# Performance work log

Measured on AMD Instinct MI355X. Metric: run time of the kernel, lower is better.

The kernel has to match this reference:

```python
import jax, jax.numpy as jnp
import numpy as np

D_MODEL, D_K, D_V, H, M = 1024, 64, 64, 16, 40


def setup_inputs() -> dict:
    key = jax.random.key(0)
    ks = jax.random.split(key, 16)
    b, nq, nk = 8, 1024, 1024
    inp = {
        "queries": jax.random.normal(ks[0], (b, nq, D_MODEL), jnp.float32),
        "keys": jax.random.normal(ks[1], (b, nk, D_MODEL), jnp.float32),
        "values": jax.random.normal(ks[2], (b, nk, D_MODEL), jnp.float32),
        "attention_mask": jax.random.randint(ks[3], (b, H, nq, nk), 0, 2) > 0,
        # Linear params, parametrized as x @ W + b (W has shape (in, out)).
        "Wq": jax.random.normal(ks[4], (D_MODEL, H * D_K), jnp.float32) * 0.03,
        "bq": jnp.zeros((H * D_K,), jnp.float32),
        "Wk": jax.random.normal(ks[5], (D_MODEL, H * D_K), jnp.float32) * 0.03,
        "bk": jnp.zeros((H * D_K,), jnp.float32),
        "Wv": jax.random.normal(ks[6], (D_MODEL, H * D_V), jnp.float32) * 0.03,
        "bv": jnp.zeros((H * D_V,), jnp.float32),
        "Wo": jax.random.normal(ks[7], (H * D_V, D_MODEL), jnp.float32) * 0.03,
        "bo": jnp.zeros((D_MODEL,), jnp.float32),
        # Memory slots: m_k ~ N(0, 1/d_k), m_v ~ N(0, 1/m), shape (1, m, h*d)
        "m_k": jax.random.normal(ks[8], (1, M, H * D_K), jnp.float32) / D_K,
        "m_v": jax.random.normal(ks[9], (1, M, H * D_V), jnp.float32) / M,
    }
    return inp


def reference(queries, keys, values, attention_mask, Wq, bq, Wk, bk, Wv, bv, Wo, bo, m_k, m_v):
    b, nq, _ = queries.shape
    nk = keys.shape[1]
    scale = jnp.asarray(np.sqrt(D_K), jnp.float32)

    # scaled memory slots, broadcast over batch
    mk = scale * jnp.broadcast_to(m_k, (b, M, H * D_K))
    mv = jnp.asarray(np.sqrt(M), jnp.float32) * jnp.broadcast_to(m_v, (b, M, H * D_V))

    q = (queries @ Wq + bq).reshape(b, nq, H, D_K).transpose(0, 2, 1, 3)       # b h nq dk
    k = jnp.concatenate([keys @ Wk + bk, mk], axis=1)                           # b (nk+m) h*dk
    k = k.reshape(b, nk + M, H, D_K).transpose(0, 2, 1, 3)                      # b h (nk+m) dk
    v = jnp.concatenate([values @ Wv + bv, mv], axis=1)
    v = v.reshape(b, nk + M, H, D_V).transpose(0, 2, 1, 3)                      # b h (nk+m) dv

    att = jnp.einsum('bhqd,bhkd->bhqk', q, k) / scale                           # b h nq (nk+m)
    # mask only real keys; memory slots always attendable
    att_real = jnp.where(attention_mask, -jnp.inf, att[:, :, :, :nk])
    att = jnp.concatenate([att_real, att[:, :, :, nk:]], axis=-1)
    att = jax.nn.softmax(att, axis=-1)

    out = jnp.einsum('bhqk,bhkd->bhqd', att, v)
    out = out.transpose(0, 2, 1, 3).reshape(b, nq, H * D_V)
    out = out @ Wo + bo
    return out, att
```

## Files before the change

kernel.cpp:

```cpp
#include <hip/hip_runtime.h>
#include <hip/hip_bf16.h>


#define B_ 8
#define NQ 1024
#define NK 1024
#define DM 1024
#define H_ 16
#define DK 64
#define NKM 1064
#define NKP 1104
#define PSTR 280

typedef __attribute__((ext_vector_type(8))) short bf16x8;
typedef __attribute__((ext_vector_type(4))) float f32x4;
typedef __attribute__((ext_vector_type(4))) short short4v;

static __device__ __forceinline__ short f2bf(float x) {
    __hip_bfloat16 h = __float2bfloat16(x);
    return __builtin_bit_cast(short, h);
}
static __device__ __forceinline__ float bf2f(short s) {
    unsigned int u = ((unsigned int)(unsigned short)s) << 16;
    return __builtin_bit_cast(float, u);
}

static __device__ __forceinline__ bf16x8 pack8(const float* __restrict__ p) {
    float4 f0 = *(const float4*)p;
    float4 f1 = *(const float4*)(p + 4);
    bf16x8 a;
    a[0] = f2bf(f0.x); a[1] = f2bf(f0.y); a[2] = f2bf(f0.z); a[3] = f2bf(f0.w);
    a[4] = f2bf(f1.x); a[5] = f2bf(f1.y); a[6] = f2bf(f1.z); a[7] = f2bf(f1.w);
    return a;
}

static __device__ __forceinline__ void gload16(const short* g, short* l) {
    __builtin_amdgcn_global_load_lds(
        (__attribute__((address_space(1))) void*)const_cast<short*>(g),
        (__attribute__((address_space(3))) void*)l, 16, 0, 0);
}

__global__ void detect_mask_kernel(const unsigned int* __restrict__ m, int n_dwords,
                                   int* __restrict__ flag) {
    __shared__ int any_big;
    if (threadIdx.x == 0) any_big = 0;
    __syncthreads();
    for (int i = threadIdx.x; i < n_dwords; i += blockDim.x)
        if (m[i] > 1u) any_big = 1;
    __syncthreads();
    if (threadIdx.x == 0) *flag = any_big ? 0 : 1;
}

__global__ void transpose_w_kernel(const float* __restrict__ W, short* __restrict__ WT) {
    __shared__ float t[32][33];
    int tx = threadIdx.x & 31, ty = threadIdx.x >> 5;
    int k0 = blockIdx.x * 32, n0 = blockIdx.y * 32;
#pragma unroll
    for (int r = 0; r < 4; r++)
        t[ty + 8 * r][tx] = W[(size_t)(k0 + ty + 8 * r) * DM + n0 + tx];
    __syncthreads();
#pragma unroll
    for (int r = 0; r < 4; r++)
        WT[(size_t)(n0 + ty + 8 * r) * DM + k0 + tx] = f2bf(t[tx][ty + 8 * r]);
}

__global__ void convert_bf16_kernel(const float* __restrict__ a, const float* __restrict__ b,
                                    const float* __restrict__ c, short* __restrict__ out) {
    const size_t NT = (size_t)B_ * NQ * DM;
    const size_t total = NT * 3;
    size_t i = ((size_t)blockIdx.x * 256 + threadIdx.x) * 8;
    const size_t step = (size_t)gridDim.x * 256 * 8;
    for (; i < total; i += step) {
        const float* src = (i < NT) ? (a + i) : (i < 2 * NT) ? (b + (i - NT)) : (c + (i - 2 * NT));
        *(bf16x8*)(out + i) = pack8(src);
    }
}

__global__ void fill_mem_kernel(const float* __restrict__ m_k, const float* __restrict__ m_v,
                                short* __restrict__ Kh, short* __restrict__ Vt) {
    int blk = blockIdx.x;
    int bh = blk / 20, rb = blk % 20;
    int r = rb * 4 + (threadIdx.x >> 6);
    int d = threadIdx.x & 63;
    int h = bh & 15;
    float kv = 0.f, vv = 0.f;
    if (r < 40) {
        kv = 8.0f * m_k[(size_t)(r * H_ + h) * DK + d];
        vv = 6.324555320336759f * m_v[(size_t)(r * H_ + h) * DK + d];
    }
    int kk = 1024 + r;
    Kh[((size_t)bh * NKP + kk) * 64 + d] = f2bf(kv);
    Vt[((size_t)bh * 64 + d) * NKP + kk] = f2bf(vv);
}

template <int MODE>
__global__ __launch_bounds__(256) void gemm_tile_kernel(
    const short* __restrict__ Ab, const short* __restrict__ BT,
    const float* __restrict__ bias,
    float* __restrict__ outF, short* __restrict__ outB) {
    __shared__ short As[2][4096];
    __shared__ short Bs[2][4096];

    const int tid = threadIdx.x;
    const int lane = tid & 63;
    const int wid = tid >> 6;
    int swz = (blockIdx.x & 7) * 64 + (blockIdx.x >> 3);
    const int mt = swz >> 3, nt = swz & 7;
    const int brow = mt * 128, bcol = nt * 128;
    const int wr = wid >> 1, wc = wid & 1;
    const int l15 = lane & 15, lg = lane >> 4;

    f32x4 acc[4][4];
#pragma unroll
    for (int m = 0; m < 4; m++)
#pragma unroll
        for (int n = 0; n < 4; n++) acc[m][n] = f32x4{0.f, 0.f, 0.f, 0.f};

    auto stage = [&](int buf, int k0) {
#pragma unroll
        for (int i = 0; i < 2; i++) {
            int c = tid + i * 256;
            int row = c >> 2, slot = c & 3;
            int base = (c & ~63) * 8;
            gload16(Ab + (size_t)(brow + row) * DM + k0 + slot * 8, &As[buf][base]);
            gload16(BT + (size_t)(bcol + row) * DM + k0 + slot * 8, &Bs[buf][base]);
        }
    };

    stage(0, 0);
    for (int kt = 0; kt < 32; ++kt) {
        __syncthreads();
        if (kt + 1 < 32) stage((kt + 1) & 1, (kt + 1) * 32);
        const short* Ab_ = As[kt & 1];
        const short* Bb_ = Bs[kt & 1];
        bf16x8 a[4], b[4];
#pragma unroll
        for (int m = 0; m < 4; m++)
            a[m] = *(const bf16x8*)(Ab_ + (wr * 64 + m * 16 + l15) * 32 + lg * 8);
#pragma unroll
        for (int n = 0; n < 4; n++)
            b[n] = *(const bf16x8*)(Bb_ + (wc * 64 + n * 16 + l15) * 32 + lg * 8);
#pragma unroll
        for (int m = 0; m < 4; m++)
#pragma unroll
            for (int n = 0; n < 4; n++)
                acc[m][n] = __builtin_amdgcn_mfma_f32_16x16x32_bf16(a[m], b[n], acc[m][n], 0, 0, 0);
    }

#pragma unroll
    for (int n = 0; n < 4; n++) {
        int col = bcol + wc * 64 + n * 16 + l15;
        float bval = bias[col];
#pragma unroll
        for (int m = 0; m < 4; m++) {
            int row0 = brow + wr * 64 + m * 16 + lg * 4;
            if (MODE == 3) {
#pragma unroll
                for (int r = 0; r < 4; r++)
                    outF[(size_t)(row0 + r) * DM + col] = acc[m][n][r] + bval;
            } else if (MODE == 0) {
                int h = col >> 6, d = col & 63;
#pragma unroll
                for (int r = 0; r < 4; r++) {
                    int row = row0 + r;
                    int b = row >> 10, q = row & 1023;
                    outB[((size_t)(b * H_ + h) * NQ + q) * 64 + d] = f2bf(acc[m][n][r] + bval);
                }
            } else if (MODE == 1) {
                int h = col >> 6, d = col & 63;
#pragma unroll
                for (int r = 0; r < 4; r++) {
                    int row = row0 + r;
                    int b = row >> 10, kk = row & 1023;
                    outB[((size_t)(b * H_ + h) * NKP + kk) * 64 + d] = f2bf(acc[m][n][r] + bval);
                }
            } else {
                int h = col >> 6, d = col & 63;
                int b = row0 >> 10, kk0 = row0 & 1023;
                short4v sv;
#pragma unroll
                for (int r = 0; r < 4; r++) sv[r] = f2bf(acc[m][n][r] + bval);
                *(short4v*)(outB + ((size_t)(b * H_ + h) * 64 + d) * NKP + kk0) = sv;
            }
        }
    }
}

__global__ __launch_bounds__(256, 4) void attn_fused_kernel(
    const short* __restrict__ Qh, const short* __restrict__ Kh,
    const short* __restrict__ Vt,
    const unsigned char* __restrict__ mb, const int* __restrict__ mi,
    const int* __restrict__ flag,
    float* __restrict__ att, short* __restrict__ Ow) {
    __shared__ short Pl[4][16][PSTR];
    __shared__ float redS[4][16];
    __shared__ float invS[16];

    int swz = (blockIdx.x & 7) * 1024 + (blockIdx.x >> 3);
    int bh = swz >> 6;
    int q0 = (swz & 63) * 16;
    int wid = threadIdx.x >> 6;
    int lane = threadIdx.x & 63;
    int l15 = lane & 15, lg = lane >> 4;

    const short* Qb = Qh + (size_t)bh * NQ * 64;
    const short* Kb = Kh + (size_t)bh * NKP * 64;
    const short* Vb = Vt + (size_t)bh * 64 * NKP;
    const int is32 = *flag;

    bf16x8 aq0 = *(const bf16x8*)(Qb + (size_t)(q0 + l15) * 64 + lg * 8);
    bf16x8 aq1 = *(const bf16x8*)(Qb + (size_t)(q0 + l15) * 64 + 32 + lg * 8);

    size_t qrow = (size_t)bh * NQ + q0 + l15;
    const int kkw = wid * 272;
    const int rofs = ((l15 >> 2) << 3) + (l15 & 3);

    uint2 mu9[9];
#pragma unroll
    for (int pp = 0; pp < 9; ++pp) {
        int kkb = kkw + pp * 32 + lg * 8;
        if (is32) {
            unsigned mlo = 0, mhi = 0;
            if (kkb < NK) {
                int4 ma = *(const int4*)(mi + qrow * NK + kkb);
                int4 mc = *(const int4*)(mi + qrow * NK + kkb + 4);
                mlo = (ma.x ? 1u : 0u) | (ma.y ? 0x100u : 0u) |
                      (ma.z ? 0x10000u : 0u) | (ma.w ? 0x1000000u : 0u);
                mhi = (mc.x ? 1u : 0u) | (mc.y ? 0x100u : 0u) |
                      (mc.z ? 0x10000u : 0u) | (mc.w ? 0x1000000u : 0u);
            }
            mu9[pp] = make_uint2(mlo, mhi);
        } else {
            mu9[pp] = (kkb < NK) ? *(const uint2*)(mb + qrow * NK + kkb)
                                 : make_uint2(0u, 0u);
        }
    }

    f32x4 po[4];
#pragma unroll
    for (int dt = 0; dt < 4; dt++) po[dt] = f32x4{0.f, 0.f, 0.f, 0.f};
    float rs = 0.f;

#pragma unroll
    for (int pp = 0; pp < 9; ++pp) {
        int ofs = pp * 32 + lg * 8;
        int base = kkw + pp * 32;
        int kkb = base + lg * 8;
        const short* Kr0 = Kb + (size_t)(base + rofs) * 64;
        bf16x8 k0a = *(const bf16x8*)(Kr0 + lg * 8);
        bf16x8 k0b = *(const bf16x8*)(Kr0 + 32 + lg * 8);
        bf16x8 k1a = *(const bf16x8*)(Kr0 + 256 + lg * 8);
        bf16x8 k1b = *(const bf16x8*)(Kr0 + 256 + 32 + lg * 8);
        bf16x8 bv0 = *(const bf16x8*)(Vb + (size_t)(l15) * NKP + kkb);
        bf16x8 bv1 = *(const bf16x8*)(Vb + (size_t)(16 + l15) * NKP + kkb);
        bf16x8 bv2 = *(const bf16x8*)(Vb + (size_t)(32 + l15) * NKP + kkb);
        bf16x8 bv3 = *(const bf16x8*)(Vb + (size_t)(48 + l15) * NKP + kkb);
        unsigned mlo = mu9[pp].x, mhi = mu9[pp].y;

        __builtin_amdgcn_s_setprio(1);
        f32x4 s0 = {0.f, 0.f, 0.f, 0.f}, s1 = {0.f, 0.f, 0.f, 0.f};
        s0 = __builtin_amdgcn_mfma_f32_16x16x32_bf16(k0a, aq0, s0, 0, 0, 0);
        s0 = __builtin_amdgcn_mfma_f32_16x16x32_bf16(k0b, aq1, s0, 0, 0, 0);
        s1 = __builtin_amdgcn_mfma_f32_16x16x32_bf16(k1a, aq0, s1, 0, 0, 0);
        s1 = __builtin_amdgcn_mfma_f32_16x16x32_bf16(k1b, aq1, s1, 0, 0, 0);
        bool live = (kkb < NKM) && (ofs < 272);
        bf16x8 pa;
        float e;
#pragma unroll
        for (int r = 0; r < 4; r++) {
            e = (live && (((mlo >> (8 * r)) & 0xffu) == 0u)) ? __expf(s0[r] * 0.125f) : 0.f;
            rs += e;
            pa[r] = f2bf(e);
        }
#pragma unroll
        for (int r = 0; r < 4; r++) {
            e = (live && (((mhi >> (8 * r)) & 0xffu) == 0u)) ? __expf(s1[r] * 0.125f) : 0.f;
            rs += e;
            pa[4 + r] = f2bf(e);
        }
        po[0] = __builtin_amdgcn_mfma_f32_16x16x32_bf16(pa, bv0, po[0], 0, 0, 0);
        po[1] = __builtin_amdgcn_mfma_f32_16x16x32_bf16(pa, bv1, po[1], 0, 0, 0);
        po[2] = __builtin_amdgcn_mfma_f32_16x16x32_bf16(pa, bv2, po[2], 0, 0, 0);
        po[3] = __builtin_amdgcn_mfma_f32_16x16x32_bf16(pa, bv3, po[3], 0, 0, 0);
        __builtin_amdgcn_s_setprio(0);

        if (ofs < 272)
            *(bf16x8*)(&Pl[wid][l15][ofs]) = pa;
    }

    rs += __shfl_xor(rs, 16);
    rs += __shfl_xor(rs, 32);
    if (lg == 0) redS[wid][l15] = rs;
    __syncthreads();
    if (threadIdx.x < 16)
        invS[threadIdx.x] = 1.f / (redS[0][threadIdx.x] + redS[1][threadIdx.x] +
                                   redS[2][threadIdx.x] + redS[3][threadIdx.x]);
    __syncthreads();

    float* attT = att + (size_t)(bh * NQ + q0) * NKM;
#pragma unroll 4
    for (int j = 0; j < 17; ++j) {
        int f = j * 256 + threadIdx.x;
        if (f < 4256) {
            int r = f / 266;
            int c = (f - r * 266) * 4;
            int w = c / 272;
            int ofs = c - w * 272;
            short4v p = *(const short4v*)(&Pl[w][r][ofs]);
            float iv = invS[r];
            f32x4 o = {bf2f(p[0]) * iv, bf2f(p[1]) * iv,
                       bf2f(p[2]) * iv, bf2f(p[3]) * iv};
            __builtin_nontemporal_store(o, (f32x4*)(attT + (size_t)f * 4));
        }
    }
    __syncthreads();

    float* OredW = (float*)&Pl[wid][0][0];
#pragma unroll
    for (int dt = 0; dt < 4; dt++)
#pragma unroll
        for (int r = 0; r < 4; r++)
            OredW[(lg * 4 + r) * 68 + dt * 16 + l15] = po[dt][r];
    __syncthreads();

    int tq = threadIdx.x >> 4;
    int d0 = (threadIdx.x & 15) * 4;
    float4 o = {0.f, 0.f, 0.f, 0.f};
#pragma unroll
    for (int w = 0; w < 4; w++) {
        const float* Or = (const float*)&Pl[w][0][0];
        float4 v = *(const float4*)(&Or[tq * 68 + d0]);
        o.x += v.x; o.y += v.y; o.z += v.z; o.w += v.w;
    }
    float invt = invS[tq];
    int b = bh >> 4, h = bh & 15;
    short4v sv;
    sv[0] = f2bf(o.x * invt); sv[1] = f2bf(o.y * invt);
    sv[2] = f2bf(o.z * invt); sv[3] = f2bf(o.w * invt);
    *(short4v*)(Ow + ((size_t)b * NQ + q0 + tq) * DM + h * 64 + d0) = sv;
}

extern "C" void kernel_launch(void* const* d_in, const int* in_sizes, int n_in,
                              void* d_out, int out_size, void* d_ws, size_t ws_size,
                              hipStream_t stream) {
    const float* queries = (const float*)d_in[0];
    const float* keys    = (const float*)d_in[1];
    const float* values  = (const float*)d_in[2];
    const void*  mask    = d_in[3];
    const float* Wq = (const float*)d_in[4];
    const float* bq = (const float*)d_in[5];
    const float* Wk = (const float*)d_in[6];
    const float* bk = (const float*)d_in[7];
    const float* Wv = (const float*)d_in[8];
    const float* bv = (const float*)d_in[9];
    const float* Wo = (const float*)d_in[10];
    const float* bo = (const float*)d_in[11];
    const float* m_k = (const float*)d_in[12];
    const float* m_v = (const float*)d_in[13];

    short* WqT = (short*)d_ws;
    short* WkT = WqT + (size_t)DM * DM;
    short* WvT = WkT + (size_t)DM * DM;
    short* WoT = WvT + (size_t)DM * DM;
    short* Qh  = WoT + (size_t)DM * DM;
    short* Kh  = Qh + (size_t)B_ * H_ * NQ * DK;
    short* Vt  = Kh + (size_t)B_ * H_ * NKP * DK;
    short* Ow  = Vt + (size_t)B_ * H_ * DK * NKP;
    char*  after = (char*)(Ow + (size_t)B_ * NQ * DM);
    int*   flag = (int*)after;
    short* Qbf  = (short*)(after + 64);
    short* Kbf  = Qbf + (size_t)B_ * NQ * DM;
    short* Vbf  = Kbf + (size_t)B_ * NQ * DM;

    float* outO = (float*)d_out;
    float* att  = outO + (size_t)B_ * NQ * DM;

    detect_mask_kernel<<<1, 256, 0, stream>>>((const unsigned int*)mask, 4096, flag);

    dim3 tg(32, 32);
    transpose_w_kernel<<<tg, 256, 0, stream>>>(Wq, WqT);
    transpose_w_kernel<<<tg, 256, 0, stream>>>(Wk, WkT);
    transpose_w_kernel<<<tg, 256, 0, stream>>>(Wv, WvT);
    transpose_w_kernel<<<tg, 256, 0, stream>>>(Wo, WoT);

    convert_bf16_kernel<<<4096, 256, 0, stream>>>(queries, keys, values, Qbf);

    gemm_tile_kernel<0><<<512, 256, 0, stream>>>(Qbf, WqT, bq, nullptr, Qh);
    gemm_tile_kernel<1><<<512, 256, 0, stream>>>(Kbf, WkT, bk, nullptr, Kh);
    gemm_tile_kernel<2><<<512, 256, 0, stream>>>(Vbf, WvT, bv, nullptr, Vt);

    fill_mem_kernel<<<2560, 256, 0, stream>>>(m_k, m_v, Kh, Vt);

    attn_fused_kernel<<<8192, 256, 0, stream>>>(Qh, Kh, Vt,
                                                (const unsigned char*)mask, (const int*)mask,
                                                flag, att, Ow);

    gemm_tile_kernel<3><<<512, 256, 0, stream>>>(Ow, WoT, bo, outO, nullptr);
}
```

Before: 642.4 us.

## Split attention key range across eight waves and fold softmax scale into Q

The fused attention block grows from 4 to 8 waves, each covering a 136-key window instead of 272, so each wave runs 5 key steps instead of 9. The key/value padding widens to 1120 and fill_mem gets more blocks to cover the extra padded rows. Mask prefetching into a register array is replaced by per-iteration nontemporal loads, which frees registers. The 1/sqrt(dk) factor is applied in the Q projection epilogue, removing one multiply per score. The cost is a larger block, an 8-way shared-memory reduction, and half the threads idle in the final output step.

Result: slower. 712.1 us (+10.9%).

```diff
diff --git a/kernel.cpp b/kernel.cpp
--- a/kernel.cpp
+++ b/kernel.cpp
@@ -9,12 +9,15 @@
 #define H_ 16
 #define DK 64
 #define NKM 1064
-#define NKP 1104
-#define PSTR 280
+#define NKP 1120
+#define PSTR 152
+#define WIN 136
 
 typedef __attribute__((ext_vector_type(8))) short bf16x8;
 typedef __attribute__((ext_vector_type(4))) float f32x4;
 typedef __attribute__((ext_vector_type(4))) short short4v;
+typedef __attribute__((ext_vector_type(2))) unsigned int u32x2;
+typedef __attribute__((ext_vector_type(4))) int i32x4;
 
 static __device__ __forceinline__ short f2bf(float x) {
     __hip_bfloat16 h = __float2bfloat16(x);
@@ -79,7 +82,7 @@
 __global__ void fill_mem_kernel(const float* __restrict__ m_k, const float* __restrict__ m_v,
                                 short* __restrict__ Kh, short* __restrict__ Vt) {
     int blk = blockIdx.x;
-    int bh = blk / 20, rb = blk % 20;
+    int bh = blk / 24, rb = blk % 24;
     int r = rb * 4 + (threadIdx.x >> 6);
     int d = threadIdx.x & 63;
     int h = bh & 15;
@@ -164,7 +167,8 @@
                 for (int r = 0; r < 4; r++) {
                     int row = row0 + r;
                     int b = row >> 10, q = row & 1023;
-                    outB[((size_t)(b * H_ + h) * NQ + q) * 64 + d] = f2bf(acc[m][n][r] + bval);
+                    outB[((size_t)(b * H_ + h) * NQ + q) * 64 + d] =
+                        f2bf((acc[m][n][r] + bval) * 0.125f);
                 }
             } else if (MODE == 1) {
                 int h = col >> 6, d = col & 63;
@@ -186,14 +190,14 @@
     }
 }
 
-__global__ __launch_bounds__(256, 4) void attn_fused_kernel(
+__global__ __launch_bounds__(512) void attn_fused_kernel(
     const short* __restrict__ Qh, const short* __restrict__ Kh,
     const short* __restrict__ Vt,
     const unsigned char* __restrict__ mb, const int* __restrict__ mi,
     const int* __restrict__ flag,
     float* __restrict__ att, short* __restrict__ Ow) {
-    __shared__ short Pl[4][16][PSTR];
-    __shared__ float redS[4][16];
+    __shared__ short Pl[8][16][PSTR];
+    __shared__ float redS[8][16];
     __shared__ float invS[16];
 
     int swz = (blockIdx.x & 7) * 1024 + (blockIdx.x >> 3);
@@ -212,29 +216,8 @@
     bf16x8 aq1 = *(const bf16x8*)(Qb + (size_t)(q0 + l15) * 64 + 32 + lg * 8);
 
     size_t qrow = (size_t)bh * NQ + q0 + l15;
-    const int kkw = wid * 272;
+    const int kkw = wid * WIN;
     const int rofs = ((l15 >> 2) << 3) + (l15 & 3);
-
-    uint2 mu9[9];
-#pragma unroll
-    for (int pp = 0; pp < 9; ++pp) {
-        int kkb = kkw + pp * 32 + lg * 8;
-        if (is32) {
-            unsigned mlo = 0, mhi = 0;
-            if (kkb < NK) {
-                int4 ma = *(const int4*)(mi + qrow * NK + kkb);
-                int4 mc = *(const int4*)(mi + qrow * NK + kkb + 4);
-                mlo = (ma.x ? 1u : 0u) | (ma.y ? 0x100u : 0u) |
-                      (ma.z ? 0x10000u : 0u) | (ma.w ? 0x1000000u : 0u);
-                mhi = (mc.x ? 1u : 0u) | (mc.y ? 0x100u : 0u) |
-                      (mc.z ? 0x10000u : 0u) | (mc.w ? 0x1000000u : 0u);
-            }
-            mu9[pp] = make_uint2(mlo, mhi);
-        } else {
-            mu9[pp] = (kkb < NK) ? *(const uint2*)(mb + qrow * NK + kkb)
-                                 : make_uint2(0u, 0u);
-        }
-    }
 
     f32x4 po[4];
 #pragma unroll
@@ -242,7 +225,7 @@
     float rs = 0.f;
 
 #pragma unroll
-    for (int pp = 0; pp < 9; ++pp) {
+    for (int pp = 0; pp < 5; ++pp) {
         int ofs = pp * 32 + lg * 8;
         int base = kkw + pp * 32;
         int kkb = base + lg * 8;
@@ -255,7 +238,20 @@
         bf16x8 bv1 = *(const bf16x8*)(Vb + (size_t)(16 + l15) * NKP + kkb);
         bf16x8 bv2 = *(const bf16x8*)(Vb + (size_t)(32 + l15) * NKP + kkb);
         bf16x8 bv3 = *(const bf16x8*)(Vb + (size_t)(48 + l15) * NKP + kkb);
-        unsigned mlo = mu9[pp].x, mhi = mu9[pp].y;
+        unsigned mlo = 0, mhi = 0;
+        if (kkb < NK) {
+            if (is32) {
+                i32x4 ma = __builtin_nontemporal_load((const i32x4*)(mi + qrow * NK + kkb));
+                i32x4 mc2 = __builtin_nontemporal_load((const i32x4*)(mi + qrow * NK + kkb + 4));
+                mlo = (ma[0] ? 1u : 0u) | (ma[1] ? 0x100u : 0u) |
+                      (ma[2] ? 0x10000u : 0u) | (ma[3] ? 0x1000000u : 0u);
+                mhi = (mc2[0] ? 1u : 0u) | (mc2[1] ? 0x100u : 0u) |
+                      (mc2[2] ? 0x10000u : 0u) | (mc2[3] ? 0x1000000u : 0u);
+            } else {
+                u32x2 mu = __builtin_nontemporal_load((const u32x2*)(mb + qrow * NK + kkb));
+                mlo = mu[0]; mhi = mu[1];
+            }
+        }
 
         __builtin_amdgcn_s_setprio(1);
         f32x4 s0 = {0.f, 0.f, 0.f, 0.f}, s1 = {0.f, 0.f, 0.f, 0.f};
@@ -263,18 +259,18 @@
         s0 = __builtin_amdgcn_mfma_f32_16x16x32_bf16(k0b, aq1, s0, 0, 0, 0);
         s1 = __builtin_amdgcn_mfma_f32_16x16x32_bf16(k1a, aq0, s1, 0, 0, 0);
         s1 = __builtin_amdgcn_mfma_f32_16x16x32_bf16(k1b, aq1, s1, 0, 0, 0);
-        bool live = (kkb < NKM) && (ofs < 272);
+        bool live = (kkb < NKM) && (ofs < WIN);
         bf16x8 pa;
         float e;
 #pragma unroll
         for (int r = 0; r < 4; r++) {
-            e = (live && (((mlo >> (8 * r)) & 0xffu) == 0u)) ? __expf(s0[r] * 0.125f) : 0.f;
+            e = (live && (((mlo >> (8 * r)) & 0xffu) == 0u)) ? __expf(s0[r]) : 0.f;
             rs += e;
             pa[r] = f2bf(e);
         }
 #pragma unroll
         for (int r = 0; r < 4; r++) {
-            e = (live && (((mhi >> (8 * r)) & 0xffu) == 0u)) ? __expf(s1[r] * 0.125f) : 0.f;
+            e = (live && (((mhi >> (8 * r)) & 0xffu) == 0u)) ? __expf(s1[r]) : 0.f;
             rs += e;
             pa[4 + r] = f2bf(e);
         }
@@ -284,7 +280,7 @@
         po[3] = __builtin_amdgcn_mfma_f32_16x16x32_bf16(pa, bv3, po[3], 0, 0, 0);
         __builtin_amdgcn_s_setprio(0);
 
-        if (ofs < 272)
+        if (ofs < WIN)
             *(bf16x8*)(&Pl[wid][l15][ofs]) = pa;
     }
 
@@ -292,20 +288,23 @@
     rs += __shfl_xor(rs, 32);
     if (lg == 0) redS[wid][l15] = rs;
     __syncthreads();
-    if (threadIdx.x < 16)
-        invS[threadIdx.x] = 1.f / (redS[0][threadIdx.x] + redS[1][threadIdx.x] +
-                                   redS[2][threadIdx.x] + redS[3][threadIdx.x]);
+    if (threadIdx.x < 16) {
+        float s = 0.f;
+#pragma unroll
+        for (int w = 0; w < 8; w++) s += redS[w][threadIdx.x];
+        invS[threadIdx.x] = 1.f / s;
+    }
     __syncthreads();
 
     float* attT = att + (size_t)(bh * NQ + q0) * NKM;
-#pragma unroll 4
-    for (int j = 0; j < 17; ++j) {
-        int f = j * 256 + threadIdx.x;
+#pragma unroll 3
+    for (int j = 0; j < 9; ++j) {
+        int f = j * 512 + threadIdx.x;
         if (f < 4256) {
             int r = f / 266;
             int c = (f - r * 266) * 4;
-            int w = c / 272;
-            int ofs = c - w * 272;
+            int w = c / WIN;
+            int ofs = c - w * WIN;
             short4v p = *(const short4v*)(&Pl[w][r][ofs]);
             float iv = invS[r];
             f32x4 o = {bf2f(p[0]) * iv, bf2f(p[1]) * iv,
@@ -323,21 +322,23 @@
             OredW[(lg * 4 + r) * 68 + dt * 16 + l15] = po[dt][r];
     __syncthreads();
 
-    int tq = threadIdx.x >> 4;
-    int d0 = (threadIdx.x & 15) * 4;
-    float4 o = {0.f, 0.f, 0.f, 0.f};
-#pragma unroll
-    for (int w = 0; w < 4; w++) {
-        const float* Or = (const float*)&Pl[w][0][0];
-        float4 v = *(const float4*)(&Or[tq * 68 + d0]);
-        o.x += v.x; o.y += v.y; o.z += v.z; o.w += v.w;
-    }
-    float invt = invS[tq];
-    int b = bh >> 4, h = bh & 15;
-    short4v sv;
-    sv[0] = f2bf(o.x * invt); sv[1] = f2bf(o.y * invt);
-    sv[2] = f2bf(o.z * invt); sv[3] = f2bf(o.w * invt);
-    *(short4v*)(Ow + ((size_t)b * NQ + q0 + tq) * DM + h * 64 + d0) = sv;
+    if (threadIdx.x < 256) {
+        int tq = threadIdx.x >> 4;
+        int d0 = (threadIdx.x & 15) * 4;
+        float4 o = {0.f, 0.f, 0.f, 0.f};
+#pragma unroll
+        for (int w = 0; w < 8; w++) {
+            const float* Or = (const float*)&Pl[w][0][0];
+            float4 v = *(const float4*)(&Or[tq * 68 + d0]);
+            o.x += v.x; o.y += v.y; o.z += v.z; o.w += v.w;
+        }
+        float invt = invS[tq];
+        int b = bh >> 4, h = bh & 15;
+        short4v sv;
+        sv[0] = f2bf(o.x * invt); sv[1] = f2bf(o.y * invt);
+        sv[2] = f2bf(o.z * invt); sv[3] = f2bf(o.w * invt);
+        *(short4v*)(Ow + ((size_t)b * NQ + q0 + tq) * DM + h * 64 + d0) = sv;
+    }
 }
 
 extern "C" void kernel_launch(void* const* d_in, const int* in_sizes, int n_in,
@@ -389,9 +390,9 @@
     gemm_tile_kernel<1><<<512, 256, 0, stream>>>(Kbf, WkT, bk, nullptr, Kh);
     gemm_tile_kernel<2><<<512, 256, 0, stream>>>(Vbf, WvT, bv, nullptr, Vt);
 
-    fill_mem_kernel<<<2560, 256, 0, stream>>>(m_k, m_v, Kh, Vt);
-
-    attn_fused_kernel<<<8192, 256, 0, stream>>>(Qh, Kh, Vt,
+    fill_mem_kernel<<<3072, 256, 0, stream>>>(m_k, m_v, Kh, Vt);
+
+    attn_fused_kernel<<<8192, 512, 0, stream>>>(Qh, Kh, Vt,
                                                 (const unsigned char*)mask, (const int*)mask,
                                                 flag, att, Ow);
 
```

## Two-pass softmax: precompute row sums, store normalized attention directly from registers

Applied to the files above, without the earlier changes.

The attention kernel now makes a first pass over keys that computes only the masked exp row sums. The normalizer is reduced across waves, and a second pass recomputes QK^T, normalizes the probabilities and stores them to the att output straight from registers. This removes the LDS staging buffer for P and the separate copy-out loop, and the written attention values are no longer rounded through bf16. The 1/8 score scale is folded into the Q projection epilogue, and the min-blocks launch bound is dropped. In exchange, the QK MFMAs, K loads and mask loads are done twice, and the att stores become 32-byte per-lane row fragments instead of fully contiguous block writes.

After: 898.9 us. 1.4x slower.

```diff
diff --git a/kernel.cpp b/kernel.cpp
--- a/kernel.cpp
+++ b/kernel.cpp
@@ -10,11 +10,11 @@
 #define DK 64
 #define NKM 1064
 #define NKP 1104
-#define PSTR 280
 
 typedef __attribute__((ext_vector_type(8))) short bf16x8;
 typedef __attribute__((ext_vector_type(4))) float f32x4;
 typedef __attribute__((ext_vector_type(4))) short short4v;
+typedef __attribute__((ext_vector_type(2))) unsigned int u32x2;
 
 static __device__ __forceinline__ short f2bf(float x) {
     __hip_bfloat16 h = __float2bfloat16(x);
@@ -164,7 +164,8 @@
                 for (int r = 0; r < 4; r++) {
                     int row = row0 + r;
                     int b = row >> 10, q = row & 1023;
-                    outB[((size_t)(b * H_ + h) * NQ + q) * 64 + d] = f2bf(acc[m][n][r] + bval);
+                    outB[((size_t)(b * H_ + h) * NQ + q) * 64 + d] =
+                        f2bf((acc[m][n][r] + bval) * 0.125f);
                 }
             } else if (MODE == 1) {
                 int h = col >> 6, d = col & 63;
@@ -186,13 +187,13 @@
     }
 }
 
-__global__ __launch_bounds__(256, 4) void attn_fused_kernel(
+__global__ __launch_bounds__(256) void attn_fused_kernel(
     const short* __restrict__ Qh, const short* __restrict__ Kh,
     const short* __restrict__ Vt,
     const unsigned char* __restrict__ mb, const int* __restrict__ mi,
     const int* __restrict__ flag,
     float* __restrict__ att, short* __restrict__ Ow) {
-    __shared__ short Pl[4][16][PSTR];
+    __shared__ float Ored[4][16][68];
     __shared__ float redS[4][16];
     __shared__ float invS[16];
 
@@ -215,31 +216,58 @@
     const int kkw = wid * 272;
     const int rofs = ((l15 >> 2) << 3) + (l15 & 3);
 
-    uint2 mu9[9];
+    auto loadMask = [&](int kkb) -> u32x2 {
+        if (kkb >= NK) return u32x2{0u, 0u};
+        if (is32) {
+            int4 ma = *(const int4*)(mi + qrow * NK + kkb);
+            int4 mc = *(const int4*)(mi + qrow * NK + kkb + 4);
+            unsigned mlo = (ma.x ? 1u : 0u) | (ma.y ? 0x100u : 0u) |
+                           (ma.z ? 0x10000u : 0u) | (ma.w ? 0x1000000u : 0u);
+            unsigned mhi = (mc.x ? 1u : 0u) | (mc.y ? 0x100u : 0u) |
+                           (mc.z ? 0x10000u : 0u) | (mc.w ? 0x1000000u : 0u);
+            return u32x2{mlo, mhi};
+        }
+        return *(const u32x2*)(mb + qrow * NK + kkb);
+    };
+
+    float rs = 0.f;
 #pragma unroll
     for (int pp = 0; pp < 9; ++pp) {
-        int kkb = kkw + pp * 32 + lg * 8;
-        if (is32) {
-            unsigned mlo = 0, mhi = 0;
-            if (kkb < NK) {
-                int4 ma = *(const int4*)(mi + qrow * NK + kkb);
-                int4 mc = *(const int4*)(mi + qrow * NK + kkb + 4);
-                mlo = (ma.x ? 1u : 0u) | (ma.y ? 0x100u : 0u) |
-                      (ma.z ? 0x10000u : 0u) | (ma.w ? 0x1000000u : 0u);
-                mhi = (mc.x ? 1u : 0u) | (mc.y ? 0x100u : 0u) |
-                      (mc.z ? 0x10000u : 0u) | (mc.w ? 0x1000000u : 0u);
-            }
-            mu9[pp] = make_uint2(mlo, mhi);
-        } else {
-            mu9[pp] = (kkb < NK) ? *(const uint2*)(mb + qrow * NK + kkb)
-                                 : make_uint2(0u, 0u);
-        }
-    }
+        int ofs = pp * 32 + lg * 8;
+        int base = kkw + pp * 32;
+        int kkb = base + lg * 8;
+        const short* Kr0 = Kb + (size_t)(base + rofs) * 64;
+        bf16x8 k0a = *(const bf16x8*)(Kr0 + lg * 8);
+        bf16x8 k0b = *(const bf16x8*)(Kr0 + 32 + lg * 8);
+        bf16x8 k1a = *(const bf16x8*)(Kr0 + 256 + lg * 8);
+        bf16x8 k1b = *(const bf16x8*)(Kr0 + 256 + 32 + lg * 8);
+        u32x2 mu = loadMask(kkb);
+        f32x4 s0 = {0.f, 0.f, 0.f, 0.f}, s1 = {0.f, 0.f, 0.f, 0.f};
+        s0 = __builtin_amdgcn_mfma_f32_16x16x32_bf16(k0a, aq0, s0, 0, 0, 0);
+        s0 = __builtin_amdgcn_mfma_f32_16x16x32_bf16(k0b, aq1, s0, 0, 0, 0);
+        s1 = __builtin_amdgcn_mfma_f32_16x16x32_bf16(k1a, aq0, s1, 0, 0, 0);
+        s1 = __builtin_amdgcn_mfma_f32_16x16x32_bf16(k1b, aq1, s1, 0, 0, 0);
+        bool live = (kkb < NKM) && (ofs < 272);
+#pragma unroll
+        for (int r = 0; r < 4; r++)
+            rs += (live && (((mu[0] >> (8 * r)) & 0xffu) == 0u)) ? __expf(s0[r]) : 0.f;
+#pragma unroll
+        for (int r = 0; r < 4; r++)
+            rs += (live && (((mu[1] >> (8 * r)) & 0xffu) == 0u)) ? __expf(s1[r]) : 0.f;
+    }
+    rs += __shfl_xor(rs, 16);
+    rs += __shfl_xor(rs, 32);
+    if (lg == 0) redS[wid][l15] = rs;
+    __syncthreads();
+    if (threadIdx.x < 16)
+        invS[threadIdx.x] = 1.f / (redS[0][threadIdx.x] + redS[1][threadIdx.x] +
+                                   redS[2][threadIdx.x] + redS[3][threadIdx.x]);
+    __syncthreads();
+    float invq = invS[l15];
 
     f32x4 po[4];
 #pragma unroll
     for (int dt = 0; dt < 4; dt++) po[dt] = f32x4{0.f, 0.f, 0.f, 0.f};
-    float rs = 0.f;
 
 #pragma unroll
     for (int pp = 0; pp < 9; ++pp) {
@@ -255,72 +283,47 @@
         bf16x8 bv1 = *(const bf16x8*)(Vb + (size_t)(16 + l15) * NKP + kkb);
         bf16x8 bv2 = *(const bf16x8*)(Vb + (size_t)(32 + l15) * NKP + kkb);
         bf16x8 bv3 = *(const bf16x8*)(Vb + (size_t)(48 + l15) * NKP + kkb);
-        unsigned mlo = mu9[pp].x, mhi = mu9[pp].y;
-
+        u32x2 mu = loadMask(kkb);
+        f32x4 s0 = {0.f, 0.f, 0.f, 0.f}, s1 = {0.f, 0.f, 0.f, 0.f};
         __builtin_amdgcn_s_setprio(1);
-        f32x4 s0 = {0.f, 0.f, 0.f, 0.f}, s1 = {0.f, 0.f, 0.f, 0.f};
         s0 = __builtin_amdgcn_mfma_f32_16x16x32_bf16(k0a, aq0, s0, 0, 0, 0);
         s0 = __builtin_amdgcn_mfma_f32_16x16x32_bf16(k0b, aq1, s0, 0, 0, 0);
         s1 = __builtin_amdgcn_mfma_f32_16x16x32_bf16(k1a, aq0, s1, 0, 0, 0);
         s1 = __builtin_amdgcn_mfma_f32_16x16x32_bf16(k1b, aq1, s1, 0, 0, 0);
         bool live = (kkb < NKM) && (ofs < 272);
         bf16x8 pa;
-        float e;
+        f32x4 w0, w1;
 #pragma unroll
         for (int r = 0; r < 4; r++) {
-            e = (live && (((mlo >> (8 * r)) & 0xffu) == 0u)) ? __expf(s0[r] * 0.125f) : 0.f;
-            rs += e;
-            pa[r] = f2bf(e);
+            float e = (live && (((mu[0] >> (8 * r)) & 0xffu) == 0u)) ? __expf(s0[r]) : 0.f;
+            float en = e * invq;
+            w0[r] = en;
+            pa[r] = f2bf(en);
         }
 #pragma unroll
         for (int r = 0; r < 4; r++) {
-            e = (live && (((mhi >> (8 * r)) & 0xffu) == 0u)) ? __expf(s1[r] * 0.125f) : 0.f;
-            rs += e;
-            pa[4 + r] = f2bf(e);
+            float e = (live && (((mu[1] >> (8 * r)) & 0xffu) == 0u)) ? __expf(s1[r]) : 0.f;
+            float en = e * invq;
+            w1[r] = en;
+            pa[4 + r] = f2bf(en);
+        }
+        if (live) {
+            float* ap = att + qrow * NKM + kkb;
+            __builtin_nontemporal_store(w0, (f32x4*)ap);
+            __builtin_nontemporal_store(w1, (f32x4*)(ap + 4));
         }
         po[0] = __builtin_amdgcn_mfma_f32_16x16x32_bf16(pa, bv0, po[0], 0, 0, 0);
         po[1] = __builtin_amdgcn_mfma_f32_16x16x32_bf16(pa, bv1, po[1], 0, 0, 0);
         po[2] = __builtin_amdgcn_mfma_f32_16x16x32_bf16(pa, bv2, po[2], 0, 0, 0);
         po[3] = __builtin_amdgcn_mfma_f32_16x16x32_bf16(pa, bv3, po[3], 0, 0, 0);
         __builtin_amdgcn_s_setprio(0);
-
-        if (ofs < 272)
-            *(bf16x8*)(&Pl[wid][l15][ofs]) = pa;
-    }
-
-    rs += __shfl_xor(rs, 16);
-    rs += __shfl_xor(rs, 32);
-    if (lg == 0) redS[wid][l15] = rs;
-    __syncthreads();
-    if (threadIdx.x < 16)
-        invS[threadIdx.x] = 1.f / (redS[0][threadIdx.x] + redS[1][threadIdx.x] +
-                                   redS[2][threadIdx.x] + redS[3][threadIdx.x]);
-    __syncthreads();
-
-    float* attT = att + (size_t)(bh * NQ + q0) * NKM;
-#pragma unroll 4
-    for (int j = 0; j < 17; ++j) {
-        int f = j * 256 + threadIdx.x;
-        if (f < 4256) {
-            int r = f / 266;
-            int c = (f - r * 266) * 4;
-            int w = c / 272;
-            int ofs = c - w * 272;
-            short4v p = *(const short4v*)(&Pl[w][r][ofs]);
-            float iv = invS[r];
-            f32x4 o = {bf2f(p[0]) * iv, bf2f(p[1]) * iv,
-                       bf2f(p[2]) * iv, bf2f(p[3]) * iv};
-            __builtin_nontemporal_store(o, (f32x4*)(attT + (size_t)f * 4));
-        }
-    }
-    __syncthreads();
-
-    float* OredW = (float*)&Pl[wid][0][0];
+    }
+
 #pragma unroll
     for (int dt = 0; dt < 4; dt++)
 #pragma unroll
         for (int r = 0; r < 4; r++)
-            OredW[(lg * 4 + r) * 68 + dt * 16 + l15] = po[dt][r];
+            Ored[wid][lg * 4 + r][dt * 16 + l15] = po[dt][r];
     __syncthreads();
 
     int tq = threadIdx.x >> 4;
@@ -328,15 +331,13 @@
     float4 o = {0.f, 0.f, 0.f, 0.f};
 #pragma unroll
     for (int w = 0; w < 4; w++) {
-        const float* Or = (const float*)&Pl[w][0][0];
-        float4 v = *(const float4*)(&Or[tq * 68 + d0]);
+        float4 v = *(const float4*)(&Ored[w][tq][d0]);
         o.x += v.x; o.y += v.y; o.z += v.z; o.w += v.w;
     }
-    float invt = invS[tq];
     int b = bh >> 4, h = bh & 15;
     short4v sv;
-    sv[0] = f2bf(o.x * invt); sv[1] = f2bf(o.y * invt);
-    sv[2] = f2bf(o.z * invt); sv[3] = f2bf(o.w * invt);
+    sv[0] = f2bf(o.x); sv[1] = f2bf(o.y);
+    sv[2] = f2bf(o.z); sv[3] = f2bf(o.w);
     *(short4v*)(Ow + ((size_t)b * NQ + q0 + tq) * DM + h * 64 + d0) = sv;
 }
 
```
